# Performance work log

Hardware: AMD Instinct MI355X
Metric: run time of the kernel (lower is better)

## Reference

```python
import jax, jax.numpy as jnp
import numpy as np


def setup_inputs() -> dict:
    key = jax.random.key(0)
    k1, k2 = jax.random.split(key)
    B, H, S, D = 2, 16, 2048, 64
    scores = jax.random.normal(k1, (B, H, S, S), dtype=jnp.float32)
    v = jax.random.normal(k2, (B, H, S, D), dtype=jnp.float32)
    return {"scores": scores, "v": v}


def reference(scores, v):
    # softmax over last dim of [B,H,S,S], then contract with V [B,H,S,D]
    prob = jax.nn.softmax(scores, axis=-1)
    return jnp.einsum('bhqk,bhkd->bhqd', prob, v)
```

## Files before the change

### kernel.cpp

```cpp
#include <hip/hip_runtime.h>
#include <hip/hip_bf16.h>

#define NBH     32
#define SEQ     2048
#define DIM     64
#define QBLK    64
#define KBLK    256
#define NCHUNK  (SEQ / KBLK)
#define PSTR    264

typedef __attribute__((ext_vector_type(4))) float f32x4;
typedef __attribute__((ext_vector_type(8))) short bf16x8;

__device__ __forceinline__ unsigned short bfbits(float f) {
    return __builtin_bit_cast(unsigned short, __float2bfloat16(f));
}

__global__ __launch_bounds__(256)
void vprep_kernel(const float* __restrict__ v, unsigned short* __restrict__ wsv)
{
    const int blk = blockIdx.x;
    const int bh  = blk >> 5, tau = blk & 31;
    const float* vp = v + ((size_t)bh * SEQ + tau * 64) * DIM;
    unsigned short* op = wsv + (size_t)blk * 4096;

    for (int fl = threadIdx.x; fl < 512; fl += 256) {
        const int ks = fl >> 8, dt = (fl >> 6) & 3, lane = fl & 63;
        const int g = lane >> 4, c = lane & 15;
        const float* sp = vp + (ks * 32 + g * 8) * DIM + dt * 16 + c;
        bf16x8 frag;
#pragma unroll
        for (int j = 0; j < 8; ++j)
            frag[j] = (short)bfbits(sp[j * DIM]);
        *reinterpret_cast<bf16x8*>(op + fl * 8) = frag;
    }
}

__global__ __launch_bounds__(256, 2)
void softmaxv_kernel(const float* __restrict__ scores,
                     const unsigned short* __restrict__ vfrags,
                     float* __restrict__ out)
{
    __shared__ unsigned short p_lds[4][2][16 * PSTR];

    const int tid  = threadIdx.x;
    const int w    = tid >> 6;
    const int lane = tid & 63;
    const int g    = lane >> 4;
    const int c    = lane & 15;

    const int bid = blockIdx.x;
    const int nb  = (bid & 7) * 128 + (bid >> 3);
    const int bh  = nb >> 5;
    const int qb  = nb & 31;
    const int q0  = qb * QBLK;

    const float* sp = scores + ((size_t)bh * SEQ + q0 + w * 16) * SEQ + lane * 4;
    const unsigned short* vb = vfrags + (size_t)bh * 32 * 4096 + lane * 8;

    unsigned short* pb0 = &p_lds[w][0][0];
    unsigned short* pb1 = &p_lds[w][1][0];

    f32x4 acc[4];
#pragma unroll
    for (int dt = 0; dt < 4; ++dt) acc[dt] = (f32x4)0.0f;
    f32x4 accl = (f32x4)0.0f;
    bf16x8 ones;
#pragma unroll
    for (int j = 0; j < 8; ++j) ones[j] = (short)0x3F80;

    f32x4 sA[16], sB[16];
    bf16x8 vf[2][4];

#define SLOADS(dst, t)                                                         \
    {                                                                          \
        _Pragma("unroll")                                                      \
        for (int j = 0; j < 16; ++j)                                           \
            dst[j] = *reinterpret_cast<const f32x4*>(                          \
                sp + (size_t)j * SEQ + (t) * KBLK);                            \
    }

#define VLOAD(tau)                                                             \
    {                                                                          \
        _Pragma("unroll")                                                      \
        for (int ks = 0; ks < 2; ++ks)                                         \
            _Pragma("unroll")                                                  \
            for (int dt = 0; dt < 4; ++dt)                                     \
                vf[ks][dt] = *reinterpret_cast<const bf16x8*>(                 \
                    vb + (size_t)(tau) * 4096 + (ks * 4 + dt) * 512);          \
    }

#define HALF(pbuf, half)                                                       \
    {                                                                          \
        _Pragma("unroll")                                                      \
        for (int ks = 0; ks < 2; ++ks) {                                       \
            const bf16x8 a = *reinterpret_cast<const bf16x8*>(                 \
                &pbuf[c * PSTR + (half) * 64 + ks * 32 + g * 8]);              \
            _Pragma("unroll")                                                  \
            for (int dt = 0; dt < 4; ++dt)                                     \
                acc[dt] = __builtin_amdgcn_mfma_f32_16x16x32_bf16(             \
                    a, vf[ks][dt], acc[dt], 0, 0, 0);                          \
            accl = __builtin_amdgcn_mfma_f32_16x16x32_bf16(                    \
                a, ones, accl, 0, 0, 0);                                       \
        }                                                                      \
    }

#define CHUNK(cur, nxt, t, pbuf, LAST)                                         \
    {                                                                          \
        VLOAD(4 * (t))                                                         \
        if (!(LAST)) SLOADS(nxt, (t) + 1)                                      \
        _Pragma("unroll")                                                      \
        for (int j = 0; j < 16; ++j) {                                         \
            f32x4 s4 = cur[j];                                                 \
            float p0 = __expf(s4[0]);                                          \
            float p1 = __expf(s4[1]);                                          \
            float p2 = __expf(s4[2]);                                          \
            float p3 = __expf(s4[3]);                                          \
            unsigned lo = (unsigned)bfbits(p0) | ((unsigned)bfbits(p1) << 16); \
            unsigned hi = (unsigned)bfbits(p2) | ((unsigned)bfbits(p3) << 16); \
            *reinterpret_cast<uint2*>(&pbuf[j * PSTR + lane * 4]) =            \
                make_uint2(lo, hi);                                            \
        }                                                                      \
        HALF(pbuf, 0)                                                          \
        VLOAD(4 * (t) + 1)                                                     \
        HALF(pbuf, 1)                                                          \
        VLOAD(4 * (t) + 2)                                                     \
        HALF(pbuf, 2)                                                          \
        VLOAD(4 * (t) + 3)                                                     \
        HALF(pbuf, 3)                                                          \
    }

    SLOADS(sA, 0)
    for (int t = 0; t < NCHUNK; t += 2) {
        CHUNK(sA, sB, t, pb0, 0)
        CHUNK(sB, sA, t + 1, pb1, (t + 1 == NCHUNK - 1))
    }
#undef SLOADS
#undef VLOAD
#undef HALF
#undef CHUNK

    float rl[4];
#pragma unroll
    for (int r = 0; r < 4; ++r)
        rl[r] = 1.0f / accl[r];

    float* op = out + ((size_t)bh * SEQ + q0 + w * 16) * DIM;
#pragma unroll
    for (int dt = 0; dt < 4; ++dt)
#pragma unroll
        for (int r = 0; r < 4; ++r)
            op[(g * 4 + r) * DIM + dt * 16 + c] = acc[dt][r] * rl[r];
}

extern "C" void kernel_launch(void* const* d_in, const int* in_sizes, int n_in,
                              void* d_out, int out_size, void* d_ws, size_t ws_size,
                              hipStream_t stream)
{
    const float* scores = (const float*)d_in[0];
    const float* v      = (const float*)d_in[1];
    float* out          = (float*)d_out;
    unsigned short* wsv = (unsigned short*)d_ws;

    vprep_kernel<<<dim3(NBH * 32), dim3(256), 0, stream>>>(v, wsv);
    softmaxv_kernel<<<dim3(NBH * (SEQ / QBLK)), dim3(256), 0, stream>>>(scores, wsv, out);
}
```

Before: 140.1 us.

## Split work by output column tile across waves with block-shared LDS probability panels

Waves no longer each own 16 query rows over all D columns. The whole block now streams each 16-row group of scores as full 2048-wide rows (8 floats per thread, a 4-deep load ring), exponentiates them into a shared LDS panel, and after a barrier each wave computes one 16-column slice of D. This cuts the per-wave V fragment loads fourfold and makes the score reads fully contiguous per row. In exchange it adds two block barriers per row tile, stops overlapping score loads with MFMA work across chunks, and computes the row-sum MFMA redundantly in every wave.

```diff
diff --git a/kernel.cpp b/kernel.cpp
--- a/kernel.cpp
+++ b/kernel.cpp
@@ -1,19 +1,21 @@
 #include <hip/hip_runtime.h>
 #include <hip/hip_bf16.h>
 
-#define NBH     32
-#define SEQ     2048
-#define DIM     64
-#define QBLK    64
-#define KBLK    256
-#define NCHUNK  (SEQ / KBLK)
-#define PSTR    264
+#define NBH   32
+#define SEQ   2048
+#define DIM   64
+#define QBLK  64
+#define PCOLS 136
 
 typedef __attribute__((ext_vector_type(4))) float f32x4;
 typedef __attribute__((ext_vector_type(8))) short bf16x8;
+typedef __attribute__((ext_vector_type(4))) unsigned int u32x4;
 
 __device__ __forceinline__ unsigned short bfbits(float f) {
     return __builtin_bit_cast(unsigned short, __float2bfloat16(f));
+}
+__device__ __forceinline__ unsigned pk(float a, float b) {
+    return (unsigned)bfbits(a) | ((unsigned)bfbits(b) << 16);
 }
 
 __global__ __launch_bounds__(256)
@@ -41,7 +43,7 @@
                      const unsigned short* __restrict__ vfrags,
                      float* __restrict__ out)
 {
-    __shared__ unsigned short p_lds[4][2][16 * PSTR];
+    __shared__ unsigned short panels[16][16 * PCOLS];
 
     const int tid  = threadIdx.x;
     const int w    = tid >> 6;
@@ -55,102 +57,96 @@
     const int qb  = nb & 31;
     const int q0  = qb * QBLK;
 
-    const float* sp = scores + ((size_t)bh * SEQ + q0 + w * 16) * SEQ + lane * 4;
+    const float* sbase = scores + ((size_t)bh * SEQ + q0) * SEQ + tid * 8;
     const unsigned short* vb = vfrags + (size_t)bh * 32 * 4096 + lane * 8;
 
-    unsigned short* pb0 = &p_lds[w][0][0];
-    unsigned short* pb1 = &p_lds[w][1][0];
-
-    f32x4 acc[4];
+    f32x4 acc[4], accl[4];
 #pragma unroll
-    for (int dt = 0; dt < 4; ++dt) acc[dt] = (f32x4)0.0f;
-    f32x4 accl = (f32x4)0.0f;
+    for (int rt = 0; rt < 4; ++rt) { acc[rt] = (f32x4)0.0f; accl[rt] = (f32x4)0.0f; }
     bf16x8 ones;
 #pragma unroll
     for (int j = 0; j < 8; ++j) ones[j] = (short)0x3F80;
 
-    f32x4 sA[16], sB[16];
-    bf16x8 vf[2][4];
+    f32x4 s0[4], s1[4];
 
-#define SLOADS(dst, t)                                                         \
+#define ISSUE(row)                                                             \
+    {                                                                          \
+        s0[(row) & 3] = *reinterpret_cast<const f32x4*>(                       \
+            sbase + (size_t)(row) * SEQ);                                      \
+        s1[(row) & 3] = *reinterpret_cast<const f32x4*>(                       \
+            sbase + (size_t)(row) * SEQ + 4);                                  \
+    }
+
+#define VF(dst, kk)                                                            \
     {                                                                          \
         _Pragma("unroll")                                                      \
-        for (int j = 0; j < 16; ++j)                                           \
-            dst[j] = *reinterpret_cast<const f32x4*>(                          \
-                sp + (size_t)j * SEQ + (t) * KBLK);                            \
+        for (int ks = 0; ks < 4; ++ks)                                         \
+            dst[ks] = *reinterpret_cast<const bf16x8*>(                        \
+                vb + (size_t)(2 * (kk) + (ks >> 1)) * 4096 +                   \
+                ((ks & 1) * 4 + w) * 512);                                     \
     }
 
-#define VLOAD(tau)                                                             \
+#define KSTEP(VBUF, kk)                                                        \
     {                                                                          \
         _Pragma("unroll")                                                      \
-        for (int ks = 0; ks < 2; ++ks)                                         \
-            _Pragma("unroll")                                                  \
-            for (int dt = 0; dt < 4; ++dt)                                     \
-                vf[ks][dt] = *reinterpret_cast<const bf16x8*>(                 \
-                    vb + (size_t)(tau) * 4096 + (ks * 4 + dt) * 512);          \
-    }
-
-#define HALF(pbuf, half)                                                       \
-    {                                                                          \
-        _Pragma("unroll")                                                      \
-        for (int ks = 0; ks < 2; ++ks) {                                       \
-            const bf16x8 a = *reinterpret_cast<const bf16x8*>(                 \
-                &pbuf[c * PSTR + (half) * 64 + ks * 32 + g * 8]);              \
-            _Pragma("unroll")                                                  \
-            for (int dt = 0; dt < 4; ++dt)                                     \
-                acc[dt] = __builtin_amdgcn_mfma_f32_16x16x32_bf16(             \
-                    a, vf[ks][dt], acc[dt], 0, 0, 0);                          \
-            accl = __builtin_amdgcn_mfma_f32_16x16x32_bf16(                    \
-                a, ones, accl, 0, 0, 0);                                       \
+        for (int ks = 0; ks < 4; ++ks) {                                       \
+            const bf16x8 afrag = *reinterpret_cast<const bf16x8*>(             \
+                &panels[kk][c * PCOLS + ks * 32 + g * 8]);                     \
+            acc[rt] = __builtin_amdgcn_mfma_f32_16x16x32_bf16(                 \
+                afrag, VBUF[ks], acc[rt], 0, 0, 0);                            \
+            accl[rt] = __builtin_amdgcn_mfma_f32_16x16x32_bf16(                \
+                afrag, ones, accl[rt], 0, 0, 0);                               \
         }                                                                      \
     }
 
-#define CHUNK(cur, nxt, t, pbuf, LAST)                                         \
-    {                                                                          \
-        VLOAD(4 * (t))                                                         \
-        if (!(LAST)) SLOADS(nxt, (t) + 1)                                      \
-        _Pragma("unroll")                                                      \
-        for (int j = 0; j < 16; ++j) {                                         \
-            f32x4 s4 = cur[j];                                                 \
-            float p0 = __expf(s4[0]);                                          \
-            float p1 = __expf(s4[1]);                                          \
-            float p2 = __expf(s4[2]);                                          \
-            float p3 = __expf(s4[3]);                                          \
-            unsigned lo = (unsigned)bfbits(p0) | ((unsigned)bfbits(p1) << 16); \
-            unsigned hi = (unsigned)bfbits(p2) | ((unsigned)bfbits(p3) << 16); \
-            *reinterpret_cast<uint2*>(&pbuf[j * PSTR + lane * 4]) =            \
-                make_uint2(lo, hi);                                            \
-        }                                                                      \
-        HALF(pbuf, 0)                                                          \
-        VLOAD(4 * (t) + 1)                                                     \
-        HALF(pbuf, 1)                                                          \
-        VLOAD(4 * (t) + 2)                                                     \
-        HALF(pbuf, 2)                                                          \
-        VLOAD(4 * (t) + 3)                                                     \
-        HALF(pbuf, 3)                                                          \
+#define LDS_BAR asm volatile("s_waitcnt lgkmcnt(0)\n\ts_barrier" ::: "memory");
+
+    ISSUE(0) ISSUE(1) ISSUE(2) ISSUE(3)
+
+    bf16x8 vfA[4], vfB[4];
+
+#pragma unroll
+    for (int rt = 0; rt < 4; ++rt) {
+#pragma unroll
+        for (int r = 0; r < 16; ++r) {
+            const f32x4 a = s0[r & 3], b = s1[r & 3];
+            if (rt * 16 + r + 4 < 64) ISSUE(rt * 16 + r + 4)
+            const float e0 = __expf(a[0]), e1 = __expf(a[1]);
+            const float e2 = __expf(a[2]), e3 = __expf(a[3]);
+            const float e4 = __expf(b[0]), e5 = __expf(b[1]);
+            const float e6 = __expf(b[2]), e7 = __expf(b[3]);
+            u32x4 p;
+            p[0] = pk(e0, e1); p[1] = pk(e2, e3);
+            p[2] = pk(e4, e5); p[3] = pk(e6, e7);
+            *reinterpret_cast<u32x4*>(
+                &panels[tid >> 4][r * PCOLS + (tid & 15) * 8]) = p;
+        }
+
+        LDS_BAR
+
+        VF(vfA, 0)
+#pragma unroll
+        for (int kk2 = 0; kk2 < 8; ++kk2) {
+            VF(vfB, 2 * kk2 + 1)
+            KSTEP(vfA, 2 * kk2)
+            if (kk2 < 7) VF(vfA, 2 * kk2 + 2)
+            KSTEP(vfB, 2 * kk2 + 1)
+        }
+
+        LDS_BAR
     }
+#undef ISSUE
+#undef VF
+#undef KSTEP
+#undef LDS_BAR
 
-    SLOADS(sA, 0)
-    for (int t = 0; t < NCHUNK; t += 2) {
-        CHUNK(sA, sB, t, pb0, 0)
-        CHUNK(sB, sA, t + 1, pb1, (t + 1 == NCHUNK - 1))
-    }
-#undef SLOADS
-#undef VLOAD
-#undef HALF
-#undef CHUNK
-
-    float rl[4];
+    float* op = out + ((size_t)bh * SEQ + q0) * DIM + w * 16 + c;
 #pragma unroll
-    for (int r = 0; r < 4; ++r)
-        rl[r] = 1.0f / accl[r];
-
-    float* op = out + ((size_t)bh * SEQ + q0 + w * 16) * DIM;
-#pragma unroll
-    for (int dt = 0; dt < 4; ++dt)
+    for (int rt = 0; rt < 4; ++rt) {
 #pragma unroll
         for (int r = 0; r < 4; ++r)
-            op[(g * 4 + r) * DIM + dt * 16 + c] = acc[dt][r] * rl[r];
+            op[(size_t)(rt * 16 + g * 4 + r) * DIM] = acc[rt][r] * (1.0f / accl[rt][r]);
+    }
 }
 
 extern "C" void kernel_launch(void* const* d_in, const int* in_sizes, int n_in,
```

After: 202.3 us. 44.4% more time.
